# Optimization experiments

Hardware: AMD Instinct MI355X
Metric: run time of the kernel (lower is better)

## Reference

```python
import jax, jax.numpy as jnp
import numpy as np

DIM = 768
NUM_HEADS = 12
KERNEL = 3
DILATIONS = (1, 2, 3)


def setup_inputs() -> dict:
    key = jax.random.key(0)
    k1, k2, k3, k4 = jax.random.split(key, 4)
    B, N, C = 4, 4096, DIM
    return {
        "x": jax.random.normal(k1, (B, N, C), jnp.float32),
        "w_qkv": jax.random.normal(k2, (3 * C, C), jnp.float32) * 0.02,
        "w_proj": jax.random.normal(k3, (C, C), jnp.float32) * 0.02,
        "b_proj": jax.random.normal(k4, (C,), jnp.float32) * 0.02,
    }


def _dilate_attention(q, k, v, dilation, head_dim, kernel):
    # q,k,v: [B, d, N] where d = C / num_dilation
    B, d, N = q.shape
    h = d // head_dim
    scale = head_dim ** -0.5
    qh = q.reshape(B, h, head_dim, N)
    kh = k.reshape(B, h, head_dim, N)
    vh = v.reshape(B, h, head_dim, N)
    pad = dilation * (kernel - 1) // 2

    def windows(t):
        # gather the `kernel` dilated neighbors along N with zero padding
        tp = jnp.pad(t, ((0, 0), (0, 0), (0, 0), (pad, pad)))
        return jnp.stack([tp[..., j * dilation: j * dilation + N] for j in range(kernel)], axis=3)  # [B,h,hd,kernel,N]

    k_win = windows(kh)
    v_win = windows(vh)
    scores = jnp.einsum('bhdn,bhdkn->bhnk', qh, k_win) * scale  # [B,h,N,kernel]
    # Torch nn.Unfold on the [B,d,N,1] 'image' yields kernel*kernel columns;
    # only the center width-column is real, the rest are zero padding -> score 0.
    kk = kernel * kernel
    center = (kernel - 1) // 2
    scores_full = jnp.zeros(scores.shape[:3] + (kk,), scores.dtype).at[..., center::kernel].set(scores)
    probs = jax.nn.softmax(scores_full, axis=-1)  # zero-key columns dilute the softmax, faithfully
    probs_real = probs[..., center::kernel]  # [B,h,N,kernel]; zero-key columns multiply zero values
    out = jnp.einsum('bhnk,bhdkn->bhnd', probs_real, v_win)  # [B,h,N,hd]
    return out.transpose(0, 2, 1, 3).reshape(B, N, d)


def reference(x, w_qkv, w_proj, b_proj):
    B, N, C = x.shape
    nd = len(DILATIONS)
    head_dim = C // NUM_HEADS
    # [B,N,3C] -> [B,N,3,nd,C/nd] -> [nd,3,B,C/nd,N]
    qkv = (x @ w_qkv.T).reshape(B, N, 3, nd, C // nd).transpose(3, 2, 0, 4, 1)
    outs = [_dilate_attention(qkv[i, 0], qkv[i, 1], qkv[i, 2], DILATIONS[i], head_dim, KERNEL)
            for i in range(nd)]
    xo = jnp.stack(outs, axis=2).reshape(B, N, C)  # [B,N,nd,d] -> [B,N,C]
    xo = xo @ w_proj.T + b_proj
    # matches torch return (x, x2=None, v, k, q); x2 omitted (is_decoder=False)
    return (xo, qkv[:, 2], qkv[:, 1], qkv[:, 0])
```

## Files before the change

### kernel.cpp

```cpp
#include <hip/hip_runtime.h>

typedef __attribute__((ext_vector_type(8))) short bf16x8;
typedef __attribute__((ext_vector_type(4))) float f32x4;

#define SZQKV 12582912

__device__ __forceinline__ unsigned short f2bf(float f) {
    unsigned int u = __float_as_uint(f);
    unsigned int r = (u + 0x7FFFu + ((u >> 16) & 1u)) >> 16;
    return (unsigned short)r;
}

#define GLDS16(g, l) __builtin_amdgcn_global_load_lds( \
    (const __attribute__((address_space(1))) unsigned int*)(g), \
    (__attribute__((address_space(3))) unsigned int*)(l), 16, 0, 0)

__global__ void cast_all(const float* __restrict__ x,
                         const float* __restrict__ wqkv,
                         const float* __restrict__ wproj,
                         unsigned short* __restrict__ dst) {
    const int T1 = 12582912;
    const int T2 = T1 + 1769472;
    const int T3 = T2 + 589824;
    int stride = gridDim.x * blockDim.x * 4;
    for (int base = (blockIdx.x * blockDim.x + threadIdx.x) * 4; base < T3; base += stride) {
        const float* src; int off;
        if (base < T1)      { src = x;     off = base; }
        else if (base < T2) { src = wqkv;  off = base - T1; }
        else                { src = wproj; off = base - T2; }
        float4 v = *(const float4*)(src + off);
        ushort4 o;
        o.x = f2bf(v.x); o.y = f2bf(v.y); o.z = f2bf(v.z); o.w = f2bf(v.w);
        *(ushort4*)(dst + base) = o;
    }
}

template <int MODE>
__global__ __launch_bounds__(512, 2) void gemm_big(const unsigned short* __restrict__ A,
                                                   const unsigned short* __restrict__ Bw,
                                                   const float* __restrict__ bias,
                                                   float* __restrict__ dout,
                                                   int nby) {
    __shared__ unsigned char lds8[73728];
    const int t = threadIdx.x;
    const int lane = t & 63;
    const int w = t >> 6;
    const int wm = w >> 1, wn = w & 1;

    const int cpx = gridDim.x >> 3;
    const int orig = blockIdx.x;
    const int wgid = (orig & 7) * cpx + (orig >> 3);
    const int bx = wgid / nby, by = wgid - bx * nby;
    const int m0 = bx * 256;
    const int n0 = by * 128;

    const unsigned char* Ab = (const unsigned char*)A;
    const unsigned char* Bb = (const unsigned char*)Bw;

    size_t aSrc0, aSrc1, bSrc;
    {
        int c0 = t, c1 = 512 + t;
        int r0 = c0 >> 2, p0 = (c0 & 3) << 4;
        int r1 = c1 >> 2, p1 = (c1 & 3) << 4;
        aSrc0 = (size_t)(m0 + r0) * 1536 + (p0 ^ ((r0 & 3) << 4));
        aSrc1 = (size_t)(m0 + r1) * 1536 + (p1 ^ ((r1 & 3) << 4));
        int rb = t >> 2, pb = (t & 3) << 4;
        bSrc  = (size_t)(n0 + rb) * 1536 + (pb ^ ((rb & 3) << 4));
    }

    int aOff[4], bOff[4];
#pragma unroll
    for (int mi = 0; mi < 4; ++mi) {
        int row = wm * 64 + mi * 16 + (lane & 15);
        aOff[mi] = row * 64 + ((((lane >> 4) << 4)) ^ ((row & 3) << 4));
    }
#pragma unroll
    for (int ni = 0; ni < 4; ++ni) {
        int row = wn * 64 + ni * 16 + (lane & 15);
        bOff[ni] = 16384 + row * 64 + ((((lane >> 4) << 4)) ^ ((row & 3) << 4));
    }

    f32x4 acc[4][4] = {};

#define STAGE(bi, kt) do { \
    unsigned char* dst_ = lds8 + (bi) * 24576; \
    GLDS16(Ab + aSrc0 + (size_t)(kt) * 64, dst_ + t * 16); \
    GLDS16(Ab + aSrc1 + (size_t)(kt) * 64, dst_ + 8192 + t * 16); \
    GLDS16(Bb + bSrc  + (size_t)(kt) * 64, dst_ + 16384 + t * 16); \
} while (0)

    STAGE(0, 0);
    STAGE(1, 1);
    int bi = 0;
    for (int kt = 0; kt < 24; ++kt) {
        if (kt < 22) {
            int si = bi + 2; if (si >= 3) si -= 3;
            STAGE(si, kt + 2);
            asm volatile("s_waitcnt vmcnt(6)" ::: "memory");
        } else if (kt == 22) {
            asm volatile("s_waitcnt vmcnt(3)" ::: "memory");
        } else {
            asm volatile("s_waitcnt vmcnt(0)" ::: "memory");
        }
        __builtin_amdgcn_s_barrier();
        asm volatile("" ::: "memory");
        const unsigned char* base = lds8 + bi * 24576;
        bf16x8 av[4], bv[4];
#pragma unroll
        for (int mi = 0; mi < 4; ++mi) av[mi] = *(const bf16x8*)(base + aOff[mi]);
#pragma unroll
        for (int ni = 0; ni < 4; ++ni) bv[ni] = *(const bf16x8*)(base + bOff[ni]);
#pragma unroll
        for (int mi = 0; mi < 4; ++mi)
#pragma unroll
            for (int ni = 0; ni < 4; ++ni)
                acc[mi][ni] = __builtin_amdgcn_mfma_f32_16x16x32_bf16(av[mi], bv[ni], acc[mi][ni], 0, 0, 0);
        asm volatile("s_waitcnt lgkmcnt(0)" ::: "memory");
        __builtin_amdgcn_s_barrier();
        asm volatile("" ::: "memory");
        ++bi; if (bi == 3) bi = 0;
    }
#undef STAGE

    const int crow = (lane >> 4) * 4;
    const int ccol = lane & 15;
    if (MODE == 0) {
        const int b = m0 >> 12;
        const int n_base = m0 & 4095;
#pragma unroll
        for (int mi = 0; mi < 4; ++mi) {
            int n = n_base + wm * 64 + mi * 16 + crow;
#pragma unroll
            for (int ni = 0; ni < 4; ++ni) {
                int o = n0 + wn * 64 + ni * 16 + ccol;
                int sel = o / 768;
                int rem = o - sel * 768;
                float* dst = dout + (size_t)(3 - sel) * SZQKV
                           + ((size_t)((rem >> 8) * 4 + b) * 256 + (rem & 255)) * 4096 + n;
                *(f32x4*)dst = acc[mi][ni];
            }
        }
    } else {
#pragma unroll
        for (int mi = 0; mi < 4; ++mi) {
            int m = m0 + wm * 64 + mi * 16 + crow;
#pragma unroll
            for (int ni = 0; ni < 4; ++ni) {
                int o = n0 + wn * 64 + ni * 16 + ccol;
                float bb = bias[o];
#pragma unroll
                for (int r = 0; r < 4; ++r)
                    dout[(size_t)(m + r) * 768 + o] = acc[mi][ni][r] + bb;
            }
        }
    }
}

__global__ __launch_bounds__(256, 3) void gemm_proj128(const unsigned short* __restrict__ A,
                                                       const unsigned short* __restrict__ Bw,
                                                       const float* __restrict__ bias,
                                                       float* __restrict__ dout) {
    __shared__ unsigned char lds8[49152];
    const int t = threadIdx.x;
    const int lane = t & 63;
    const int w = t >> 6;
    const int wm = w >> 1, wn = w & 1;

    const int cpx = gridDim.x >> 3;
    const int orig = blockIdx.x;
    const int wgid = (orig & 7) * cpx + (orig >> 3);
    const int bx = wgid / 6, by = wgid - bx * 6;
    const int m0 = bx * 128, n0 = by * 128;

    const unsigned char* Ab = (const unsigned char*)A;
    const unsigned char* Bb = (const unsigned char*)Bw;

    const int srow = t >> 2;
    const int sc = ((t & 3) ^ (srow & 3)) << 4;
    const size_t aBase = (size_t)(m0 + srow) * 1536 + sc;
    const size_t bBase = (size_t)(n0 + srow) * 1536 + sc;
    const int ldst = t * 16;

    const int rA = wm * 64 + (lane & 15);
    const int rB = wn * 64 + (lane & 15);
    const int xt = (((lane >> 4)) ^ (lane & 3)) << 4;

    f32x4 acc[4][4] = {};

#define STAGE(kt, bi) do { \
    unsigned char* db_ = lds8 + (bi) * 16384; \
    const size_t ko_ = (size_t)(kt) * 64; \
    GLDS16(Ab + aBase + ko_,         db_ + ldst); \
    GLDS16(Ab + aBase + ko_ + 98304, db_ + ldst + 4096); \
    GLDS16(Bb + bBase + ko_,         db_ + 8192 + ldst); \
    GLDS16(Bb + bBase + ko_ + 98304, db_ + 8192 + ldst + 4096); \
} while (0)

    STAGE(0, 0);
    STAGE(1, 1);
    int bi = 0;
    for (int kt = 0; kt < 24; ++kt) {
        if (kt < 22) {
            int si = bi + 2; if (si >= 3) si -= 3;
            STAGE(kt + 2, si);
            asm volatile("s_waitcnt vmcnt(8)" ::: "memory");
        } else if (kt == 22) {
            asm volatile("s_waitcnt vmcnt(4)" ::: "memory");
        } else {
            asm volatile("s_waitcnt vmcnt(0)" ::: "memory");
        }
        __builtin_amdgcn_s_barrier();
        asm volatile("" ::: "memory");
        const unsigned char* bufA = lds8 + bi * 16384;
        const unsigned char* bufB = bufA + 8192;
        bf16x8 av[4], bv[4];
#pragma unroll
        for (int mi = 0; mi < 4; ++mi)
            av[mi] = *(const bf16x8*)(bufA + (rA + mi * 16) * 64 + xt);
#pragma unroll
        for (int ni = 0; ni < 4; ++ni)
            bv[ni] = *(const bf16x8*)(bufB + (rB + ni * 16) * 64 + xt);
#pragma unroll
        for (int mi = 0; mi < 4; ++mi)
#pragma unroll
            for (int ni = 0; ni < 4; ++ni)
                acc[mi][ni] = __builtin_amdgcn_mfma_f32_16x16x32_bf16(av[mi], bv[ni], acc[mi][ni], 0, 0, 0);
        asm volatile("s_waitcnt lgkmcnt(0)" ::: "memory");
        __builtin_amdgcn_s_barrier();
        asm volatile("" ::: "memory");
        ++bi; if (bi == 3) bi = 0;
    }
#undef STAGE

    float* ldsf = (float*)lds8;
    const int ccol = lane & 15;
    const int hi4 = (lane >> 4) * 4;
#pragma unroll
    for (int s = 0; s < 2; ++s) {
        if (wm == s) {
#pragma unroll
            for (int mi = 0; mi < 4; ++mi)
#pragma unroll
                for (int ni = 0; ni < 4; ++ni) {
                    int o = wn * 64 + ni * 16 + ccol;
                    int m2b = mi * 16 + hi4;
#pragma unroll
                    for (int r = 0; r < 4; ++r)
                        ldsf[(m2b + r) * 128 + (o ^ (((m2b + r) & 7) << 2))] = acc[mi][ni][r];
                }
        }
        asm volatile("s_waitcnt lgkmcnt(0)" ::: "memory");
        __builtin_amdgcn_s_barrier();
        asm volatile("" ::: "memory");
#pragma unroll
        for (int it = 0; it < 8; ++it) {
            int idx = it * 256 + t;
            int row = idx >> 5;
            int c4 = (idx & 31) * 4;
            f32x4 v = *(const f32x4*)&ldsf[row * 128 + (c4 ^ ((row & 7) << 2))];
            f32x4 b4 = *(const f32x4*)(bias + n0 + c4);
            v = v + b4;
            float* dst = dout + (size_t)(m0 + s * 64 + row) * 768 + n0 + c4;
            *(f32x4*)dst = v;
        }
        if (s == 0) {
            __builtin_amdgcn_s_barrier();
            asm volatile("" ::: "memory");
        }
    }
}

__global__ __launch_bounds__(256) void attn_kernel(const float* __restrict__ qkv,
                                                   unsigned short* __restrict__ attnbf) {
    const int chunk = blockIdx.x;
    const int dil_i = blockIdx.y;
    const int b     = blockIdx.z;
    const int dil   = dil_i + 1;
    const int t  = threadIdx.x;
    const int h  = t >> 6;
    const int nl = t & 63;
    const int n  = chunk * 64 + nl;

    const size_t gb = (size_t)(dil_i * 4 + b) * 256 * 4096;
    const float* Q = qkv + (size_t)3 * SZQKV + gb;
    const float* K = qkv + (size_t)2 * SZQKV + gb;
    const float* V = qkv + (size_t)1 * SZQKV + gb;

    const int nm = n - dil, np = n + dil;
    const bool vm = (nm >= 0), vp = (np < 4096);
    const int nmc = vm ? nm : 0, npc = vp ? np : 4095;

    float s0 = 0.f, s1 = 0.f, s2 = 0.f;
    {
        const float* qrow = Q + (size_t)h * 64 * 4096;
        const float* krow = K + (size_t)h * 64 * 4096;
        for (int d = 0; d < 64; ++d) {
            float q = qrow[n];
            s0 += q * krow[nmc];
            s1 += q * krow[n];
            s2 += q * krow[npc];
            qrow += 4096; krow += 4096;
        }
    }
    s0 = vm ? s0 * 0.125f : 0.f;
    s1 *= 0.125f;
    s2 = vp ? s2 * 0.125f : 0.f;
    float mx = fmaxf(0.f, fmaxf(s0, fmaxf(s1, s2)));
    float e0 = __expf(s0 - mx), e1 = __expf(s1 - mx), e2 = __expf(s2 - mx);
    float den = e0 + e1 + e2 + 6.f * __expf(-mx);
    float inv = 1.f / den;
    float p0 = vm ? e0 * inv : 0.f;
    float p1 = e1 * inv;
    float p2 = vp ? e2 * inv : 0.f;

    __shared__ unsigned short lout[256][65];
    {
        const float* vrow = V + (size_t)h * 64 * 4096;
        for (int d = 0; d < 64; ++d) {
            float o = p0 * vrow[nmc] + p1 * vrow[n] + p2 * vrow[npc];
            lout[h * 64 + d][nl] = f2bf(o);
            vrow += 4096;
        }
    }
    __syncthreads();

#pragma unroll
    for (int i = 0; i < 8; ++i) {
        int linear = i * 256 + t;
        int nn   = linear >> 5;
        int cblk = linear & 31;
        union { unsigned short u[8]; f32x4 v; } tt;
#pragma unroll
        for (int j = 0; j < 8; ++j) tt.u[j] = lout[cblk * 8 + j][nn];
        unsigned short* dst = attnbf + (size_t)(b * 4096 + chunk * 64 + nn) * 768
                            + dil_i * 256 + cblk * 8;
        *(f32x4*)dst = tt.v;
    }
}

extern "C" void kernel_launch(void* const* d_in, const int* in_sizes, int n_in,
                              void* d_out, int out_size, void* d_ws, size_t ws_size,
                              hipStream_t stream) {
    const float* x     = (const float*)d_in[0];
    const float* wqkv  = (const float*)d_in[1];
    const float* wproj = (const float*)d_in[2];
    const float* bproj = (const float*)d_in[3];
    float* out = (float*)d_out;

    unsigned short* xbf     = (unsigned short*)d_ws;
    unsigned short* wqkvbf  = xbf + 12582912;
    unsigned short* wprojbf = wqkvbf + 1769472;
    unsigned short* attnbf  = wprojbf + 589824;

    cast_all<<<2048, 256, 0, stream>>>(x, wqkv, wproj, xbf);

    gemm_big<0><<<dim3(64 * 18), 512, 0, stream>>>(xbf, wqkvbf, nullptr, out, 18);

    attn_kernel<<<dim3(64, 3, 4), 256, 0, stream>>>(out, attnbf);

    gemm_proj128<<<dim3(768), 256, 0, stream>>>(attnbf, wprojbf, bproj, out);
}
```

Baseline: 174.7 us.

## Use 4-wave QKV GEMM blocks with 128x64 per-wave tiles and MFMA priority

The QKV projection GEMM goes from 512 threads (8 waves, 64x64 per wave) to 256 threads (4 waves, 128x64 per wave) while keeping the 256x128 block tile and triple-buffered LDS pipeline. Each wave now reuses its B fragments across twice as many A rows, which cuts LDS reads per MFMA. MFMA groups are wrapped in s_setprio to favor the math issue. In exchange each wave holds twice the accumulators, which raises register pressure, and each thread issues twice as many async global-to-LDS loads, so the vmcnt waits are adjusted to match.

```diff
diff --git a/kernel.cpp b/kernel.cpp
--- a/kernel.cpp
+++ b/kernel.cpp
@@ -35,12 +35,9 @@
     }
 }
 
-template <int MODE>
-__global__ __launch_bounds__(512, 2) void gemm_big(const unsigned short* __restrict__ A,
+__global__ __launch_bounds__(256, 2) void gemm_qkv(const unsigned short* __restrict__ A,
                                                    const unsigned short* __restrict__ Bw,
-                                                   const float* __restrict__ bias,
-                                                   float* __restrict__ dout,
-                                                   int nby) {
+                                                   float* __restrict__ dout) {
     __shared__ unsigned char lds8[73728];
     const int t = threadIdx.x;
     const int lane = t & 63;
@@ -50,43 +47,49 @@
     const int cpx = gridDim.x >> 3;
     const int orig = blockIdx.x;
     const int wgid = (orig & 7) * cpx + (orig >> 3);
-    const int bx = wgid / nby, by = wgid - bx * nby;
-    const int m0 = bx * 256;
-    const int n0 = by * 128;
+    const int bx = wgid / 18, by = wgid - bx * 18;
+    const int m0 = bx * 256, n0 = by * 128;
 
     const unsigned char* Ab = (const unsigned char*)A;
     const unsigned char* Bb = (const unsigned char*)Bw;
 
-    size_t aSrc0, aSrc1, bSrc;
-    {
-        int c0 = t, c1 = 512 + t;
-        int r0 = c0 >> 2, p0 = (c0 & 3) << 4;
-        int r1 = c1 >> 2, p1 = (c1 & 3) << 4;
-        aSrc0 = (size_t)(m0 + r0) * 1536 + (p0 ^ ((r0 & 3) << 4));
-        aSrc1 = (size_t)(m0 + r1) * 1536 + (p1 ^ ((r1 & 3) << 4));
-        int rb = t >> 2, pb = (t & 3) << 4;
-        bSrc  = (size_t)(n0 + rb) * 1536 + (pb ^ ((rb & 3) << 4));
-    }
-
-    int aOff[4], bOff[4];
-#pragma unroll
-    for (int mi = 0; mi < 4; ++mi) {
-        int row = wm * 64 + mi * 16 + (lane & 15);
-        aOff[mi] = row * 64 + ((((lane >> 4) << 4)) ^ ((row & 3) << 4));
-    }
-#pragma unroll
-    for (int ni = 0; ni < 4; ++ni) {
-        int row = wn * 64 + ni * 16 + (lane & 15);
-        bOff[ni] = 16384 + row * 64 + ((((lane >> 4) << 4)) ^ ((row & 3) << 4));
-    }
-
-    f32x4 acc[4][4] = {};
-
-#define STAGE(bi, kt) do { \
-    unsigned char* dst_ = lds8 + (bi) * 24576; \
-    GLDS16(Ab + aSrc0 + (size_t)(kt) * 64, dst_ + t * 16); \
-    GLDS16(Ab + aSrc1 + (size_t)(kt) * 64, dst_ + 8192 + t * 16); \
-    GLDS16(Bb + bSrc  + (size_t)(kt) * 64, dst_ + 16384 + t * 16); \
+    const int srow = t >> 2;
+    const int sc = ((t & 3) ^ (srow & 3)) << 4;
+    const size_t aBase = (size_t)(m0 + srow) * 1536 + sc;
+    const size_t bBase = (size_t)(n0 + srow) * 1536 + sc;
+    const int ldst = t * 16;
+
+    const int rA = wm * 128 + (lane & 15);
+    const int rB = wn * 64 + (lane & 15);
+    const int xt = (((lane >> 4)) ^ (lane & 3)) << 4;
+
+    f32x4 acc[8][4] = {};
+
+#define STAGE(kt, bi) do { \
+    unsigned char* db_ = lds8 + (bi) * 24576; \
+    const size_t ko_ = (size_t)(kt) * 64; \
+    GLDS16(Ab + aBase + ko_,          db_ + ldst); \
+    GLDS16(Ab + aBase + ko_ + 98304,  db_ + ldst + 4096); \
+    GLDS16(Ab + aBase + ko_ + 196608, db_ + ldst + 8192); \
+    GLDS16(Ab + aBase + ko_ + 294912, db_ + ldst + 12288); \
+    GLDS16(Bb + bBase + ko_,          db_ + 16384 + ldst); \
+    GLDS16(Bb + bBase + ko_ + 98304,  db_ + 16384 + ldst + 4096); \
+} while (0)
+
+#define LDA4(mb_) do { \
+    _Pragma("unroll") \
+    for (int mi = 0; mi < 4; ++mi) \
+        av[mi] = *(const bf16x8*)(bufA + (rA + (mb_) + mi * 16) * 64 + xt); \
+} while (0)
+
+#define MM(rbase_) do { \
+    __builtin_amdgcn_s_setprio(1); \
+    _Pragma("unroll") \
+    for (int mi = 0; mi < 4; ++mi) \
+    _Pragma("unroll") \
+    for (int ni = 0; ni < 4; ++ni) \
+        acc[(rbase_) + mi][ni] = __builtin_amdgcn_mfma_f32_16x16x32_bf16(av[mi], bv[ni], acc[(rbase_) + mi][ni], 0, 0, 0); \
+    __builtin_amdgcn_s_setprio(0); \
 } while (0)
 
     STAGE(0, 0);
@@ -95,63 +98,47 @@
     for (int kt = 0; kt < 24; ++kt) {
         if (kt < 22) {
             int si = bi + 2; if (si >= 3) si -= 3;
-            STAGE(si, kt + 2);
+            STAGE(kt + 2, si);
+            asm volatile("s_waitcnt vmcnt(12)" ::: "memory");
+        } else if (kt == 22) {
             asm volatile("s_waitcnt vmcnt(6)" ::: "memory");
-        } else if (kt == 22) {
-            asm volatile("s_waitcnt vmcnt(3)" ::: "memory");
         } else {
             asm volatile("s_waitcnt vmcnt(0)" ::: "memory");
         }
         __builtin_amdgcn_s_barrier();
         asm volatile("" ::: "memory");
-        const unsigned char* base = lds8 + bi * 24576;
+        const unsigned char* bufA = lds8 + bi * 24576;
+        const unsigned char* bufB = bufA + 16384;
         bf16x8 av[4], bv[4];
 #pragma unroll
-        for (int mi = 0; mi < 4; ++mi) av[mi] = *(const bf16x8*)(base + aOff[mi]);
-#pragma unroll
-        for (int ni = 0; ni < 4; ++ni) bv[ni] = *(const bf16x8*)(base + bOff[ni]);
-#pragma unroll
-        for (int mi = 0; mi < 4; ++mi)
-#pragma unroll
-            for (int ni = 0; ni < 4; ++ni)
-                acc[mi][ni] = __builtin_amdgcn_mfma_f32_16x16x32_bf16(av[mi], bv[ni], acc[mi][ni], 0, 0, 0);
+        for (int ni = 0; ni < 4; ++ni)
+            bv[ni] = *(const bf16x8*)(bufB + (rB + ni * 16) * 64 + xt);
+        LDA4(0);  MM(0);
+        LDA4(64); MM(4);
         asm volatile("s_waitcnt lgkmcnt(0)" ::: "memory");
         __builtin_amdgcn_s_barrier();
         asm volatile("" ::: "memory");
         ++bi; if (bi == 3) bi = 0;
     }
 #undef STAGE
+#undef LDA4
+#undef MM
 
     const int crow = (lane >> 4) * 4;
     const int ccol = lane & 15;
-    if (MODE == 0) {
-        const int b = m0 >> 12;
-        const int n_base = m0 & 4095;
-#pragma unroll
-        for (int mi = 0; mi < 4; ++mi) {
-            int n = n_base + wm * 64 + mi * 16 + crow;
-#pragma unroll
-            for (int ni = 0; ni < 4; ++ni) {
-                int o = n0 + wn * 64 + ni * 16 + ccol;
-                int sel = o / 768;
-                int rem = o - sel * 768;
-                float* dst = dout + (size_t)(3 - sel) * SZQKV
-                           + ((size_t)((rem >> 8) * 4 + b) * 256 + (rem & 255)) * 4096 + n;
-                *(f32x4*)dst = acc[mi][ni];
-            }
-        }
-    } else {
-#pragma unroll
-        for (int mi = 0; mi < 4; ++mi) {
-            int m = m0 + wm * 64 + mi * 16 + crow;
-#pragma unroll
-            for (int ni = 0; ni < 4; ++ni) {
-                int o = n0 + wn * 64 + ni * 16 + ccol;
-                float bb = bias[o];
-#pragma unroll
-                for (int r = 0; r < 4; ++r)
-                    dout[(size_t)(m + r) * 768 + o] = acc[mi][ni][r] + bb;
-            }
+    const int b = m0 >> 12;
+    const int n_base = m0 & 4095;
+#pragma unroll
+    for (int mi = 0; mi < 8; ++mi) {
+        int n = n_base + wm * 128 + mi * 16 + crow;
+#pragma unroll
+        for (int ni = 0; ni < 4; ++ni) {
+            int o = n0 + wn * 64 + ni * 16 + ccol;
+            int sel = o / 768;
+            int rem = o - sel * 768;
+            float* dst = dout + (size_t)(3 - sel) * SZQKV
+                       + ((size_t)((rem >> 8) * 4 + b) * 256 + (rem & 255)) * 4096 + n;
+            *(f32x4*)dst = acc[mi][ni];
         }
     }
 }
@@ -354,7 +341,7 @@
 
     cast_all<<<2048, 256, 0, stream>>>(x, wqkv, wproj, xbf);
 
-    gemm_big<0><<<dim3(64 * 18), 512, 0, stream>>>(xbf, wqkvbf, nullptr, out, 18);
+    gemm_qkv<<<dim3(1152), 256, 0, stream>>>(xbf, wqkvbf, out);
 
     attn_kernel<<<dim3(64, 3, 4), 256, 0, stream>>>(out, attnbf);
 
```

New measurement: 174.3 us. No clear change (-0.2%).
